# Performance work log

Hardware: AMD Instinct MI355X
Metric: run time of the kernel (lower is better)

The kernel has to match this reference:

```python
import jax, jax.numpy as jnp
import numpy as np

N_NODES = 20000
N_EDGES = 320000
F_IN = 256
HID = 256
N_CLS = 5


def _glorot(key, shape):
    lim = np.sqrt(6.0 / (shape[0] + shape[1]))
    return jax.random.uniform(key, shape, jnp.float32, -lim, lim)


def setup_inputs() -> dict:
    key = jax.random.key(0)
    ks = jax.random.split(key, 12)
    x1 = jax.random.normal(ks[0], (N_NODES, F_IN), jnp.float32)
    x2 = jax.random.normal(ks[1], (N_NODES, F_IN), jnp.float32)
    ei1 = jax.random.randint(ks[2], (2, N_EDGES), 0, N_NODES, jnp.int64 if jax.config.jax_enable_x64 else jnp.int32)
    ei2 = jax.random.randint(ks[3], (2, N_EDGES), 0, N_NODES, jnp.int64 if jax.config.jax_enable_x64 else jnp.int32)
    params = {
        'W1': _glorot(ks[4], (F_IN, HID)), 'b1': jnp.zeros((HID,), jnp.float32),
        'W2': _glorot(ks[5], (HID, HID)), 'b2': jnp.zeros((HID,), jnp.float32),
        'W3': _glorot(ks[6], (HID, HID)), 'b3': jnp.zeros((HID,), jnp.float32),
        'Wl': _glorot(ks[7], (HID, N_CLS)), 'bl': jnp.zeros((N_CLS,), jnp.float32),
    }
    return {'x1': x1, 'edge_index1': ei1, 'x2': x2, 'edge_index2': ei2, **params}


def gcn_conv(x, edge_index, W, b):
    # PyG GCNConv: add self-loops, symmetric normalization D^-1/2 (A+I) D^-1/2 (X W) + b
    N = x.shape[0]
    src, dst = edge_index[0], edge_index[1]
    deg = jax.ops.segment_sum(jnp.ones(src.shape[0], x.dtype), dst, num_segments=N) + 1.0
    dinv = jax.lax.rsqrt(deg)  # [N]
    xw = x @ W                 # [N, H]
    coef = (dinv[src] * dinv[dst])[:, None]  # per-edge norm
    agg = jax.ops.segment_sum(xw[src] * coef, dst, num_segments=N)
    agg = agg + xw * (dinv * dinv)[:, None]  # self-loop term
    return agg + b


def _branch(x, ei, W1, b1, W2, b2, W3, b3):
    # dropout is identity in eval mode
    h = jax.nn.relu(gcn_conv(x, ei, W1, b1))
    h = jax.nn.relu(gcn_conv(h, ei, W2, b2))
    return gcn_conv(h, ei, W3, b3)


def reference(x1, edge_index1, x2, edge_index2, W1, b1, W2, b2, W3, b3, Wl, bl):
    h1 = _branch(x1, edge_index1, W1, b1, W2, b2, W3, b3)
    h2 = _branch(x2, edge_index2, W1, b1, W2, b2, W3, b3)
    h = jnp.concatenate([h1, h2], axis=0)          # [2N, H]
    pooled = jnp.mean(h, axis=0, keepdims=True)    # batch is all zeros -> single mean pool
    return pooled @ Wl + bl                        # [1, num_classes]
```

## Files before the change

kernel.cpp:

```cpp
#include <hip/hip_runtime.h>
#include <hip/hip_bf16.h>

#define N_NODES 20000
#define N_EDGES 320000
#define HID 256

typedef __attribute__((ext_vector_type(8))) short bf16x8;
typedef __attribute__((ext_vector_type(4))) float f32x4;
typedef __attribute__((ext_vector_type(8))) unsigned short us8;

__device__ __forceinline__ float bf2f(ushort u) {
  union { unsigned int i; float f; } v; v.i = ((unsigned int)u) << 16; return v.f;
}
__device__ __forceinline__ ushort f2bf(float f) {
  union { float f; unsigned int i; } v; v.f = f;
  unsigned int r = v.i + 0x7FFFu + ((v.i >> 16) & 1u);
  return (ushort)(r >> 16);
}

__global__ void init_detect_kernel(int* cnt0, int* cnt1, float* t0, float* t1,
                                   const void* x1, const void* ei1, int* flags) {
  if (blockIdx.x == gridDim.x - 1) {
    __shared__ int cnt_wild, cnt_oddnz;
    if (threadIdx.x == 0) { cnt_wild = 0; cnt_oddnz = 0; }
    __syncthreads();
    const ushort* xu = (const ushort*)x1;
    int wild = 0;
#pragma unroll
    for (int k = 0; k < 4; k++) {
      ushort u = xu[threadIdx.x * 4 + k];
      int ex = (u >> 7) & 0xFF;
      if (ex >= 0x90) wild++;
    }
    if (wild) atomicAdd(&cnt_wild, wild);
    const int* ii = (const int*)ei1;
    if (ii[threadIdx.x * 2 + 1] != 0) atomicAdd(&cnt_oddnz, 1);
    __syncthreads();
    if (threadIdx.x == 0) {
      flags[0] = (cnt_wild > 64) ? 1 : 0;
      flags[1] = (cnt_oddnz < 8) ? 1 : 0;
    }
    return;
  }
  int i = blockIdx.x * blockDim.x + threadIdx.x;
  if (i < N_NODES) { cnt0[i] = 0; cnt1[i] = 0; t0[i] = 0.f; t1[i] = 0.f; }
}

__global__ void cvt_ei_count_kernel(const void* e0, const void* e1,
                                    int* o0, int* o1,
                                    int* cnt0, int* cnt1,
                                    int* rank0, int* rank1, const int* flags) {
  int b = blockIdx.y;
  const void* e = b ? e1 : e0;
  int* o = b ? o1 : o0;
  int* cnt = b ? cnt1 : cnt0;
  int* rank = b ? rank1 : rank0;
  int i = blockIdx.x * 256 + threadIdx.x;
  if (i >= 2 * N_EDGES) return;
  int v = flags[1] ? (int)((const long long*)e)[i] : ((const int*)e)[i];
  o[i] = v;
  if (i >= N_EDGES) rank[i - N_EDGES] = atomicAdd(&cnt[v], 1);
}

__global__ void cvt_x_kernel(const void* x0, const void* x1v,
                             ushort* o0, ushort* o1, const int* flags) {
  const void* x = blockIdx.y ? x1v : x0;
  ushort* o = blockIdx.y ? o1 : o0;
  int i4 = (blockIdx.x * 256 + threadIdx.x) * 4;
  if (i4 >= N_NODES * HID) return;
  if (flags[0]) {
    float4 v = *(const float4*)((const float*)x + i4);
    ushort4 w; w.x = f2bf(v.x); w.y = f2bf(v.y); w.z = f2bf(v.z); w.w = f2bf(v.w);
    *(ushort4*)(o + i4) = w;
  } else {
    *(ushort4*)(o + i4) = *(const ushort4*)((const ushort*)x + i4);
  }
}

__global__ void cvt_w_kernel(const void* W1, const void* W2, const void* W3, const void* Wl,
                             const void* b1, const void* b2, const void* b3, const void* bl,
                             ushort* out, const int* flags) {
  int i = blockIdx.x * 256 + threadIdx.x;
  if (i >= 198661) return;
  const void* src; int off; bool tr = false;
  if (i < 65536)       { src = W1; off = 0; tr = true; }
  else if (i < 131072) { src = W2; off = 65536; tr = true; }
  else if (i < 196608) { src = W3; off = 131072; }
  else if (i < 197888) { src = Wl; off = 196608; }
  else if (i < 198144) { src = b1; off = 197888; }
  else if (i < 198400) { src = b2; off = 198144; }
  else if (i < 198656) { src = b3; off = 198400; }
  else                 { src = bl; off = 198656; }
  int j = i - off;
  if (tr) j = (j & 255) * 256 + (j >> 8);
  out[i] = flags[0] ? f2bf(((const float*)src)[j]) : ((const ushort*)src)[j];
}

__global__ __launch_bounds__(1024) void scan_kernel(const int* cnt0, const int* cnt1,
                                                    int* rp0, int* rp1,
                                                    float* dinv0, float* dinv1) {
  const int* cnt = blockIdx.x ? cnt1 : cnt0;
  int* rp = blockIdx.x ? rp1 : rp0;
  float* dinv = blockIdx.x ? dinv1 : dinv0;
  __shared__ int sd[1024];
  int tid = threadIdx.x;
  int base = tid * 20;
  int pref[20];
  int run = 0;
#pragma unroll
  for (int k = 0; k < 20; k++) {
    int i = base + k;
    int c = (i < N_NODES) ? cnt[i] : 0;
    if (i < N_NODES) dinv[i] = rsqrtf((float)c + 1.0f);
    run += c;
    pref[k] = run;
  }
  sd[tid] = run;
  __syncthreads();
  for (int off = 1; off < 1024; off <<= 1) {
    int v = (tid >= off) ? sd[tid - off] : 0;
    __syncthreads();
    sd[tid] += v;
    __syncthreads();
  }
  int offset = sd[tid] - run;
  if (tid == 0) rp[0] = 0;
#pragma unroll
  for (int k = 0; k < 20; k++) {
    int i = base + k;
    if (i < N_NODES) rp[i + 1] = offset + pref[k];
  }
}

__global__ void fill_kernel(const int* ei0, const int* ei1,
                            const float* dinv0, const float* dinv1,
                            const int* rp0, const int* rp1,
                            const int* rank0, const int* rank1,
                            int2* eg0, int2* eg1,
                            float* t0, float* t1) {
  int e = blockIdx.x * blockDim.x + threadIdx.x;
  if (e >= N_EDGES) return;
  int b = blockIdx.y;
  const int* ei = b ? ei1 : ei0;
  const float* dinv = b ? dinv1 : dinv0;
  const int* rp = b ? rp1 : rp0;
  const int* rank = b ? rank1 : rank0;
  int2* eg = b ? eg1 : eg0;
  float* t = b ? t1 : t0;
  int src = ei[e], dst = ei[N_EDGES + e];
  int slot = rp[dst] + rank[e];
  float dd = dinv[dst];
  eg[slot] = make_int2(src, __float_as_int(dinv[src] * dd));
  atomicAdd(&t[src], dd);
}

__global__ __launch_bounds__(256) void gemm_kernel(
    const ushort* __restrict__ A0, const ushort* __restrict__ A1,
    const ushort* __restrict__ Wt,
    ushort* __restrict__ C0, ushort* __restrict__ C1) {
  const ushort* A = blockIdx.z ? A1 : A0;
  ushort* C = blockIdx.z ? C1 : C0;
  int m0 = blockIdx.x * 64;
  int n0 = blockIdx.y * 64;
  __shared__ ushort As[64][40];
  __shared__ ushort Bs[64][40];
  int tid = threadIdx.x;
  int wave = tid >> 6, lane = tid & 63;
  int quad = lane >> 4, r16 = lane & 15;
  f32x4 acc0 = {0.f, 0.f, 0.f, 0.f}, acc1 = acc0, acc2 = acc0, acc3 = acc0;
  int l_row = tid >> 2;
  int l_off = (tid & 3) * 8;
  for (int k0 = 0; k0 < 256; k0 += 32) {
    int gr = m0 + l_row;
    int4 va = {0, 0, 0, 0};
    if (gr < N_NODES) va = *(const int4*)(A + gr * 256 + k0 + l_off);
    *(int4*)&As[l_row][l_off] = va;
    int4 vb = *(const int4*)(Wt + (n0 + l_row) * 256 + k0 + l_off);
    *(int4*)&Bs[l_row][l_off] = vb;
    __syncthreads();
    bf16x8 a  = *(const bf16x8*)&As[wave * 16 + r16][quad * 8];
    bf16x8 b0 = *(const bf16x8*)&Bs[r16][quad * 8];
    bf16x8 b1 = *(const bf16x8*)&Bs[16 + r16][quad * 8];
    bf16x8 b2 = *(const bf16x8*)&Bs[32 + r16][quad * 8];
    bf16x8 b3 = *(const bf16x8*)&Bs[48 + r16][quad * 8];
    acc0 = __builtin_amdgcn_mfma_f32_16x16x32_bf16(a, b0, acc0, 0, 0, 0);
    acc1 = __builtin_amdgcn_mfma_f32_16x16x32_bf16(a, b1, acc1, 0, 0, 0);
    acc2 = __builtin_amdgcn_mfma_f32_16x16x32_bf16(a, b2, acc2, 0, 0, 0);
    acc3 = __builtin_amdgcn_mfma_f32_16x16x32_bf16(a, b3, acc3, 0, 0, 0);
    __syncthreads();
  }
  int orow = m0 + wave * 16 + quad * 4;
#pragma unroll
  for (int r = 0; r < 4; r++) {
    int gr = orow + r;
    if (gr < N_NODES) {
      ushort* cp = C + gr * 256 + n0 + r16;
      cp[0]  = f2bf(acc0[r]);
      cp[16] = f2bf(acc1[r]);
      cp[32] = f2bf(acc2[r]);
      cp[48] = f2bf(acc3[r]);
    }
  }
}

__global__ __launch_bounds__(256) void agg_kernel(
    const ushort* __restrict__ XW0, const ushort* __restrict__ XW1,
    const float* __restrict__ dinv0, const float* __restrict__ dinv1,
    const int* __restrict__ rp0, const int* __restrict__ rp1,
    const int2* __restrict__ eg0, const int2* __restrict__ eg1,
    const ushort* __restrict__ bias,
    ushort* __restrict__ H0, ushort* __restrict__ H1) {
  int shard = blockIdx.x & 7;
  int nodeblk = blockIdx.x >> 3;
  int branch = shard >> 2;
  int quarter = shard & 3;
  const ushort* XW = branch ? XW1 : XW0;
  const float* dinv = branch ? dinv1 : dinv0;
  const int* rp = branch ? rp1 : rp0;
  const int2* eg = branch ? eg1 : eg0;
  ushort* H = branch ? H1 : H0;
  int wave = threadIdx.x >> 6, lane = threadIdx.x & 63;
  int grp = lane >> 3;
  int j = lane & 7;
  int fb = quarter * 64 + j * 8;
  int i = nodeblk * 32 + wave * 8 + grp;
  float di = dinv[i];
  float selfw = di * di;
  us8 v = *(const us8*)(XW + i * 256 + fb);
  float accA[8], accB[8];
#pragma unroll
  for (int k = 0; k < 8; k++) { accA[k] = selfw * bf2f(v[k]); accB[k] = 0.f; }
  int e = rp[i], eend = rp[i + 1];
  int m = eend - e;
  m = max(m, __shfl_xor(m, 8));
  m = max(m, __shfl_xor(m, 16));
  m = max(m, __shfl_xor(m, 32));
  int trips = (m + 1) >> 1;
  for (int t = 0; t < trips; t++) {
    bool a0 = e < eend;
    bool a1 = e + 1 < eend;
    long long q0 = __builtin_nontemporal_load((const long long*)(eg + (a0 ? e : 0)));
    long long q1 = __builtin_nontemporal_load((const long long*)(eg + (a1 ? e + 1 : 0)));
    int s0 = (int)(unsigned)(unsigned long long)q0;
    int s1 = (int)(unsigned)(unsigned long long)q1;
    float w0 = a0 ? __int_as_float((int)(q0 >> 32)) : 0.f;
    float w1 = a1 ? __int_as_float((int)(q1 >> 32)) : 0.f;
    us8 r0 = *(const us8*)(XW + s0 * 256 + fb);
    us8 r1 = *(const us8*)(XW + s1 * 256 + fb);
#pragma unroll
    for (int k = 0; k < 8; k++) {
      accA[k] += w0 * bf2f(r0[k]);
      accB[k] += w1 * bf2f(r1[k]);
    }
    e += 2;
  }
  us8 bb = *(const us8*)(bias + fb);
  us8 o;
#pragma unroll
  for (int k = 0; k < 8; k++) {
    o[k] = f2bf(fmaxf(accA[k] + accB[k] + bf2f(bb[k]), 0.f));
  }
  *(us8*)(H + i * 256 + fb) = o;
}

__global__ __launch_bounds__(256) void colsum_kernel(
    const ushort* __restrict__ H0, const ushort* __restrict__ H1,
    const float* __restrict__ dinv0, const float* __restrict__ dinv1,
    const float* __restrict__ t0, const float* __restrict__ t1,
    float* __restrict__ P) {
  int b = blockIdx.y;
  const ushort* H = b ? H1 : H0;
  const float* dinv = b ? dinv1 : dinv0;
  const float* t = b ? t1 : t0;
  int wave = threadIdx.x >> 6, lane = threadIdx.x & 63;
  int wid = blockIdx.x * 4 + wave;
  int f4 = lane * 4;
  float a0 = 0.f, a1 = 0.f, a2 = 0.f, a3 = 0.f;
  for (int j = wid; j < N_NODES; j += 256) {
    float dj = dinv[j];
    float c = dj * (t[j] + dj);
    ushort4 u = *(const ushort4*)(H + j * 256 + f4);
    a0 += c * bf2f(u.x); a1 += c * bf2f(u.y);
    a2 += c * bf2f(u.z); a3 += c * bf2f(u.w);
  }
  __shared__ float part[4][256];
  part[wave][f4 + 0] = a0; part[wave][f4 + 1] = a1;
  part[wave][f4 + 2] = a2; part[wave][f4 + 3] = a3;
  __syncthreads();
  int f = threadIdx.x;
  float ssum = part[0][f] + part[1][f] + part[2][f] + part[3][f];
  P[(b * 64 + blockIdx.x) * 256 + f] = ssum;
}

__global__ __launch_bounds__(256) void final_kernel(
    const float* __restrict__ P,
    const ushort* __restrict__ W3, const ushort* __restrict__ b3,
    const ushort* __restrict__ Wl, const ushort* __restrict__ bl,
    void* __restrict__ out, const int* __restrict__ flags) {
  __shared__ float v[256];
  __shared__ float pooled[256];
  int t = threadIdx.x;
  float acc0 = 0.f, acc1 = 0.f;
  for (int b = 0; b < 64; b++) {
    acc0 += P[b * 256 + t];
    acc1 += P[(64 + b) * 256 + t];
  }
  v[t] = acc0 + acc1;
  __syncthreads();
  float acc = 0.f;
  for (int f = 0; f < 256; f++) acc += v[f] * bf2f(W3[f * 256 + t]);
  pooled[t] = acc * (1.0f / (2.0f * N_NODES)) + bf2f(b3[t]);
  __syncthreads();
  if (t < 5) {
    float o = bf2f(bl[t]);
    for (int h = 0; h < 256; h++) o += pooled[h] * bf2f(Wl[h * 5 + t]);
    if (flags[0]) ((float*)out)[t] = o;
    else ((ushort*)out)[t] = f2bf(o);
  }
}

extern "C" void kernel_launch(void* const* d_in, const int* in_sizes, int n_in,
                              void* d_out, int out_size, void* d_ws, size_t ws_size,
                              hipStream_t stream) {
  const void* x1 = d_in[0];
  const void* ei1 = d_in[1];
  const void* x2 = d_in[2];
  const void* ei2 = d_in[3];
  const void* W1 = d_in[4];
  const void* b1 = d_in[5];
  const void* W2 = d_in[6];
  const void* b2 = d_in[7];
  const void* W3 = d_in[8];
  const void* b3 = d_in[9];
  const void* Wl = d_in[10];
  const void* bl = d_in[11];

  char* p = (char*)d_ws;
  auto alloc = [&](size_t bytes) {
    char* r = p;
    p += (bytes + 255) & ~size_t(255);
    return r;
  };
  int* flags   = (int*)alloc(256);
  float* dinv0 = (float*)alloc(N_NODES * 4);
  float* dinv1 = (float*)alloc(N_NODES * 4);
  float* t0    = (float*)alloc(N_NODES * 4);
  float* t1    = (float*)alloc(N_NODES * 4);
  int* cnt0    = (int*)alloc(N_NODES * 4);
  int* cnt1    = (int*)alloc(N_NODES * 4);
  int* rp0     = (int*)alloc((N_NODES + 1) * 4);
  int* rp1     = (int*)alloc((N_NODES + 1) * 4);
  int2* eg0    = (int2*)alloc((size_t)N_EDGES * 8);
  int2* eg1    = (int2*)alloc((size_t)N_EDGES * 8);
  float* Pp    = (float*)alloc(2 * 64 * 256 * 4);
  ushort* wbuf = (ushort*)alloc(198661 * 2);
  ushort* xw0  = (ushort*)alloc((size_t)N_NODES * HID * 2);
  ushort* xw1  = (ushort*)alloc((size_t)N_NODES * HID * 2);
  ushort* xc0  = (ushort*)alloc((size_t)N_NODES * HID * 2);
  ushort* xc1  = (ushort*)alloc((size_t)N_NODES * HID * 2);
  int* ei32_0 = (int*)xw0;
  int* ei32_1 = ei32_0 + 2 * N_EDGES;
  int* rank0  = ei32_1 + 2 * N_EDGES;
  int* rank1  = rank0 + N_EDGES;
  ushort* h0 = xc0;
  ushort* h1 = xc1;

  ushort* Wc1 = wbuf + 0;
  ushort* Wc2 = wbuf + 65536;
  ushort* Wc3 = wbuf + 131072;
  ushort* Wlc = wbuf + 196608;
  ushort* bc1 = wbuf + 197888;
  ushort* bc2 = wbuf + 198144;
  ushort* bc3 = wbuf + 198400;
  ushort* blc = wbuf + 198656;

  init_detect_kernel<<<(N_NODES + 255) / 256 + 1, 256, 0, stream>>>(
      cnt0, cnt1, t0, t1, x1, ei1, flags);
  cvt_ei_count_kernel<<<dim3((2 * N_EDGES + 255) / 256, 2), 256, 0, stream>>>(
      ei1, ei2, ei32_0, ei32_1, cnt0, cnt1, rank0, rank1, flags);
  cvt_x_kernel<<<dim3(N_NODES * HID / 1024, 2), 256, 0, stream>>>(
      x1, x2, xc0, xc1, flags);
  cvt_w_kernel<<<(198661 + 255) / 256, 256, 0, stream>>>(
      W1, W2, W3, Wl, b1, b2, b3, bl, wbuf, flags);
  scan_kernel<<<2, 1024, 0, stream>>>(cnt0, cnt1, rp0, rp1, dinv0, dinv1);
  fill_kernel<<<dim3((N_EDGES + 255) / 256, 2), 256, 0, stream>>>(
      ei32_0, ei32_1, dinv0, dinv1, rp0, rp1, rank0, rank1, eg0, eg1, t0, t1);

  gemm_kernel<<<dim3(313, 4, 2), 256, 0, stream>>>(xc0, xc1, Wc1, xw0, xw1);
  agg_kernel<<<dim3(5000), 256, 0, stream>>>(
      xw0, xw1, dinv0, dinv1, rp0, rp1, eg0, eg1, bc1, h0, h1);

  gemm_kernel<<<dim3(313, 4, 2), 256, 0, stream>>>(h0, h1, Wc2, xw0, xw1);
  agg_kernel<<<dim3(5000), 256, 0, stream>>>(
      xw0, xw1, dinv0, dinv1, rp0, rp1, eg0, eg1, bc2, h0, h1);

  colsum_kernel<<<dim3(64, 2), 256, 0, stream>>>(h0, h1, dinv0, dinv1, t0, t1, Pp);
  final_kernel<<<1, 256, 0, stream>>>(Pp, Wc3, bc3, Wlc, blc, d_out, flags);
}
```

Measured before the change: 430.7 us.

## Pack edge entries to 32 bits and remap aggregation to half-wave per node

Edge records are packed into 32 bits: a 16-bit source index plus a bf16 normalisation weight, halving edge-list traffic. The aggregation kernel now gives each node a half-wave covering all 256 features, instead of splitting features into quarter shards across blocks, so each edge is read once per node rather than four times. The edge loop is unrolled by four with a scalar tail instead of a wave-max trip count with masked loads. The 16-bit index relies on the node count fitting in 16 bits, and the bf16 edge weights lose precision.

```diff
diff --git a/kernel.cpp b/kernel.cpp
--- a/kernel.cpp
+++ b/kernel.cpp
@@ -136,7 +136,7 @@
                             const float* dinv0, const float* dinv1,
                             const int* rp0, const int* rp1,
                             const int* rank0, const int* rank1,
-                            int2* eg0, int2* eg1,
+                            unsigned int* eg0, unsigned int* eg1,
                             float* t0, float* t1) {
   int e = blockIdx.x * blockDim.x + threadIdx.x;
   if (e >= N_EDGES) return;
@@ -145,12 +145,12 @@
   const float* dinv = b ? dinv1 : dinv0;
   const int* rp = b ? rp1 : rp0;
   const int* rank = b ? rank1 : rank0;
-  int2* eg = b ? eg1 : eg0;
+  unsigned int* eg = b ? eg1 : eg0;
   float* t = b ? t1 : t0;
   int src = ei[e], dst = ei[N_EDGES + e];
   int slot = rp[dst] + rank[e];
   float dd = dinv[dst];
-  eg[slot] = make_int2(src, __float_as_int(dinv[src] * dd));
+  eg[slot] = (unsigned int)src | ((unsigned int)f2bf(dinv[src] * dd) << 16);
   atomicAdd(&t[src], dd);
 }
 
@@ -207,60 +207,55 @@
     const ushort* __restrict__ XW0, const ushort* __restrict__ XW1,
     const float* __restrict__ dinv0, const float* __restrict__ dinv1,
     const int* __restrict__ rp0, const int* __restrict__ rp1,
-    const int2* __restrict__ eg0, const int2* __restrict__ eg1,
+    const unsigned int* __restrict__ eg0, const unsigned int* __restrict__ eg1,
     const ushort* __restrict__ bias,
     ushort* __restrict__ H0, ushort* __restrict__ H1) {
-  int shard = blockIdx.x & 7;
-  int nodeblk = blockIdx.x >> 3;
-  int branch = shard >> 2;
-  int quarter = shard & 3;
-  const ushort* XW = branch ? XW1 : XW0;
-  const float* dinv = branch ? dinv1 : dinv0;
-  const int* rp = branch ? rp1 : rp0;
-  const int2* eg = branch ? eg1 : eg0;
-  ushort* H = branch ? H1 : H0;
+  int b = blockIdx.y;
+  const ushort* XW = b ? XW1 : XW0;
+  const float* dinv = b ? dinv1 : dinv0;
+  const int* rp = b ? rp1 : rp0;
+  const unsigned int* eg = b ? eg1 : eg0;
+  ushort* H = b ? H1 : H0;
   int wave = threadIdx.x >> 6, lane = threadIdx.x & 63;
-  int grp = lane >> 3;
-  int j = lane & 7;
-  int fb = quarter * 64 + j * 8;
-  int i = nodeblk * 32 + wave * 8 + grp;
+  int half = lane >> 5;
+  int fl = (lane & 31) * 8;
+  int i = blockIdx.x * 8 + wave * 2 + half;
   float di = dinv[i];
   float selfw = di * di;
-  us8 v = *(const us8*)(XW + i * 256 + fb);
-  float accA[8], accB[8];
-#pragma unroll
-  for (int k = 0; k < 8; k++) { accA[k] = selfw * bf2f(v[k]); accB[k] = 0.f; }
+  us8 v = *(const us8*)(XW + i * 256 + fl);
+  float acc[8], acc2[8];
+#pragma unroll
+  for (int k = 0; k < 8; k++) { acc[k] = selfw * bf2f(v[k]); acc2[k] = 0.f; }
   int e = rp[i], eend = rp[i + 1];
-  int m = eend - e;
-  m = max(m, __shfl_xor(m, 8));
-  m = max(m, __shfl_xor(m, 16));
-  m = max(m, __shfl_xor(m, 32));
-  int trips = (m + 1) >> 1;
-  for (int t = 0; t < trips; t++) {
-    bool a0 = e < eend;
-    bool a1 = e + 1 < eend;
-    long long q0 = __builtin_nontemporal_load((const long long*)(eg + (a0 ? e : 0)));
-    long long q1 = __builtin_nontemporal_load((const long long*)(eg + (a1 ? e + 1 : 0)));
-    int s0 = (int)(unsigned)(unsigned long long)q0;
-    int s1 = (int)(unsigned)(unsigned long long)q1;
-    float w0 = a0 ? __int_as_float((int)(q0 >> 32)) : 0.f;
-    float w1 = a1 ? __int_as_float((int)(q1 >> 32)) : 0.f;
-    us8 r0 = *(const us8*)(XW + s0 * 256 + fb);
-    us8 r1 = *(const us8*)(XW + s1 * 256 + fb);
+  for (; e + 4 <= eend; e += 4) {
+    unsigned int p0 = eg[e], p1 = eg[e + 1], p2 = eg[e + 2], p3 = eg[e + 3];
+    us8 r0 = *(const us8*)(XW + (p0 & 0xFFFFu) * 256 + fl);
+    us8 r1 = *(const us8*)(XW + (p1 & 0xFFFFu) * 256 + fl);
+    us8 r2 = *(const us8*)(XW + (p2 & 0xFFFFu) * 256 + fl);
+    us8 r3 = *(const us8*)(XW + (p3 & 0xFFFFu) * 256 + fl);
+    float w0 = bf2f((ushort)(p0 >> 16)), w1 = bf2f((ushort)(p1 >> 16));
+    float w2 = bf2f((ushort)(p2 >> 16)), w3 = bf2f((ushort)(p3 >> 16));
 #pragma unroll
     for (int k = 0; k < 8; k++) {
-      accA[k] += w0 * bf2f(r0[k]);
-      accB[k] += w1 * bf2f(r1[k]);
+      acc[k]  += w0 * bf2f(r0[k]);
+      acc2[k] += w1 * bf2f(r1[k]);
+      acc[k]  += w2 * bf2f(r2[k]);
+      acc2[k] += w3 * bf2f(r3[k]);
     }
-    e += 2;
-  }
-  us8 bb = *(const us8*)(bias + fb);
+  }
+  for (; e < eend; e++) {
+    unsigned int pp = eg[e];
+    us8 r = *(const us8*)(XW + (pp & 0xFFFFu) * 256 + fl);
+    float w = bf2f((ushort)(pp >> 16));
+#pragma unroll
+    for (int k = 0; k < 8; k++) acc[k] += w * bf2f(r[k]);
+  }
+  us8 bb = *(const us8*)(bias + fl);
   us8 o;
 #pragma unroll
-  for (int k = 0; k < 8; k++) {
-    o[k] = f2bf(fmaxf(accA[k] + accB[k] + bf2f(bb[k]), 0.f));
-  }
-  *(us8*)(H + i * 256 + fb) = o;
+  for (int k = 0; k < 8; k++)
+    o[k] = f2bf(fmaxf(acc[k] + acc2[k] + bf2f(bb[k]), 0.f));
+  *(us8*)(H + i * 256 + fl) = o;
 }
 
 __global__ __launch_bounds__(256) void colsum_kernel(
@@ -350,8 +345,8 @@
   int* cnt1    = (int*)alloc(N_NODES * 4);
   int* rp0     = (int*)alloc((N_NODES + 1) * 4);
   int* rp1     = (int*)alloc((N_NODES + 1) * 4);
-  int2* eg0    = (int2*)alloc((size_t)N_EDGES * 8);
-  int2* eg1    = (int2*)alloc((size_t)N_EDGES * 8);
+  unsigned int* eg0 = (unsigned int*)alloc((size_t)N_EDGES * 4);
+  unsigned int* eg1 = (unsigned int*)alloc((size_t)N_EDGES * 4);
   float* Pp    = (float*)alloc(2 * 64 * 256 * 4);
   ushort* wbuf = (ushort*)alloc(198661 * 2);
   ushort* xw0  = (ushort*)alloc((size_t)N_NODES * HID * 2);
@@ -387,11 +382,11 @@
       ei32_0, ei32_1, dinv0, dinv1, rp0, rp1, rank0, rank1, eg0, eg1, t0, t1);
 
   gemm_kernel<<<dim3(313, 4, 2), 256, 0, stream>>>(xc0, xc1, Wc1, xw0, xw1);
-  agg_kernel<<<dim3(5000), 256, 0, stream>>>(
+  agg_kernel<<<dim3(2500, 2), 256, 0, stream>>>(
       xw0, xw1, dinv0, dinv1, rp0, rp1, eg0, eg1, bc1, h0, h1);
 
   gemm_kernel<<<dim3(313, 4, 2), 256, 0, stream>>>(h0, h1, Wc2, xw0, xw1);
-  agg_kernel<<<dim3(5000), 256, 0, stream>>>(
+  agg_kernel<<<dim3(2500, 2), 256, 0, stream>>>(
       xw0, xw1, dinv0, dinv1, rp0, rp1, eg0, eg1, bc2, h0, h1);
 
   colsum_kernel<<<dim3(64, 2), 256, 0, stream>>>(h0, h1, dinv0, dinv1, t0, t1, Pp);
```

Measured after the change: 381.2 us. 11.5% less time.
